# Kernel optimization log

Hardware: AMD Instinct MI355X
Metric: run time of the kernel (lower is better)

## Reference

```python
import jax, jax.numpy as jnp
import numpy as np

HIDDEN = 128
SEQ_LEN = 7
BATCH = 65536


def setup_inputs() -> dict:
    key = jax.random.key(0)
    ks = jax.random.split(key, 8)
    H = HIDDEN
    s = 1.0 / np.sqrt(H)  # PyTorch LSTM/Linear init range
    x = jax.random.normal(ks[0], (BATCH, SEQ_LEN, 1), dtype=jnp.float32)
    x0 = jax.random.uniform(ks[1], (BATCH, 1), dtype=jnp.float32)
    W_ih = jax.random.uniform(ks[2], (4 * H, 1), jnp.float32, -s, s)
    W_hh = jax.random.uniform(ks[3], (4 * H, H), jnp.float32, -s, s)
    b_ih = jax.random.uniform(ks[4], (4 * H,), jnp.float32, -s, s)
    b_hh = jax.random.uniform(ks[5], (4 * H,), jnp.float32, -s, s)
    W_out = jax.random.uniform(ks[6], (1, H), jnp.float32, -s, s)
    b_out = jax.random.uniform(ks[7], (1,), jnp.float32, -s, s)
    return {"x": x, "x0": x0, "W_ih": W_ih, "W_hh": W_hh,
            "b_ih": b_ih, "b_hh": b_hh, "W_out": W_out, "b_out": b_out}


def reference(x, x0, W_ih, W_hh, b_ih, b_hh, W_out, b_out):
    B, T, _ = x.shape
    H = W_hh.shape[1]
    # Step i consumes the output of the previous shift: x0, then x[:, 0..T-2]
    # (x[:, T-1] is assigned but never fed into the LSTM, matching the torch loop).
    xs = jnp.concatenate([x0[:, None, :], x[:, : T - 1, :]], axis=1)  # [B, T, 1]
    xs = jnp.swapaxes(xs, 0, 1)  # [T, B, 1] for scan

    h0 = jnp.zeros((B, H), dtype=x.dtype)
    c0 = jnp.zeros((B, H), dtype=x.dtype)
    bias = b_ih + b_hh  # [4H]

    def step(carry, x_t):
        h, c = carry
        # gates: [B, 4H]; PyTorch gate order is i, f, g, o
        gates = x_t @ W_ih.T + h @ W_hh.T + bias
        i_g, f_g, g_g, o_g = jnp.split(gates, 4, axis=-1)
        i_g = jax.nn.sigmoid(i_g)
        f_g = jax.nn.sigmoid(f_g)
        g_g = jnp.tanh(g_g)
        o_g = jax.nn.sigmoid(o_g)
        c_new = f_g * c + i_g * g_g
        h_new = o_g * jnp.tanh(c_new)
        pred = h_new @ W_out.T + b_out  # [B, 1]
        return (h_new, c_new), pred

    _, preds = jax.lax.scan(step, (h0, c0), xs)  # preds: [T, B, 1]
    return jnp.swapaxes(preds, 0, 1)  # [B, T, 1]
```

## Files before the change

### kernel.cpp

```cpp
#include <hip/hip_runtime.h>


#define SEQ 7
#define BT 32

typedef _Float16 half8 __attribute__((ext_vector_type(8)));
typedef float floatx4 __attribute__((ext_vector_type(4)));
typedef float floatx2 __attribute__((ext_vector_type(2)));

__device__ __forceinline__ floatx4 mfma16(half8 a, half8 b, floatx4 c) {
  return __builtin_amdgcn_mfma_f32_16x16x32_f16(a, b, c, 0, 0, 0);
}

#define LOG2E 1.4426950408889634f
#define K2 2.885390081777927f

__device__ __forceinline__ floatx2 pexp2m(floatx2 v) {
  floatx2 r;
  r.x = __builtin_amdgcn_exp2f(-v.x);
  r.y = __builtin_amdgcn_exp2f(-v.y);
  return r;
}
__device__ __forceinline__ floatx2 prcp(floatx2 v) {
  floatx2 r;
  r.x = __builtin_amdgcn_rcpf(v.x);
  r.y = __builtin_amdgcn_rcpf(v.y);
  return r;
}

__global__ void pack_kernel(const float* __restrict__ Whh,
                            const float* __restrict__ Wout,
                            _Float16* __restrict__ Bp) {
  int idx = blockIdx.x * 256 + threadIdx.x;
  if (idx < 65536) {
    int jj = idx & 7;
    int lane = (idx >> 3) & 63;
    int kk = (idx >> 9) & 3;
    int nt = idx >> 11;
    int g = nt >> 3, w = nt & 7;
    int col = lane & 15, quad = lane >> 4;
    int j = g * 128 + w * 16 + col;
    int k = 32 * kk + 8 * quad + jj;
    float S = (g == 2) ? K2 : LOG2E;
    Bp[idx] = (_Float16)(S * Whh[j * 128 + k]);
  } else {
    int pos = idx - 65536;
    int hl = pos >> 11;
    int e = pos & 2047;
    int jj = e & 7;
    int lane = (e >> 3) & 63;
    int kk = e >> 9;
    int col = lane & 15, quad = lane >> 4;
    int k = 32 * kk + 8 * quad + jj;
    float wv = Wout[k];
    _Float16 hi = (_Float16)wv;
    _Float16 v = hl ? (_Float16)(wv - (float)hi) : hi;
    Bp[idx] = (col == 0) ? v : (_Float16)0.0f;
  }
}

__launch_bounds__(512, 4)
__global__ void lstm_kernel(const float* __restrict__ x,
                            const float* __restrict__ x0,
                            const float* __restrict__ Wih,
                            const float* __restrict__ bih,
                            const float* __restrict__ bhh,
                            const float* __restrict__ boutp,
                            const _Float16* __restrict__ Bp,
                            float* __restrict__ out) {
  __shared__ _Float16 Ah[2][BT][136];
  __shared__ float xs[2][BT];
  __shared__ _Float16 Wo[4096];
  __shared__ float Twb[8][16][8];

  const int tid = threadIdx.x;
  const int w = tid >> 6;
  const int lane = tid & 63;
  const int col = lane & 15;
  const int quad = lane >> 4;
  const int rowbase = blockIdx.x * BT;

  ((half8*)Wo)[tid] = ((const half8*)(Bp + 65536))[tid];

  if (tid < 128) {
    int tw = tid >> 4, tc = tid & 15;
#pragma unroll
    for (int g = 0; g < 4; ++g) {
      int j = g * 128 + tw * 16 + tc;
      float S = (g == 2) ? K2 : LOG2E;
      Twb[tw][tc][g] = S * Wih[j];
      Twb[tw][tc][4 + g] = S * (bih[j] + bhh[j]);
    }
  }

  half8 bw[4][4];
#pragma unroll
  for (int g = 0; g < 4; ++g)
#pragma unroll
    for (int kk = 0; kk < 4; ++kk)
      bw[g][kk] =
          *(const half8*)(Bp + (((g * 8 + w) * 4 + kk) * 64 + lane) * 8);

  const float bout = boutp[0];

  floatx2 c2[2][2];
#pragma unroll
  for (int mt = 0; mt < 2; ++mt)
#pragma unroll
    for (int p = 0; p < 2; ++p) c2[mt][p] = (floatx2){0.f, 0.f};

  if (tid < BT) xs[0][tid] = x0[rowbase + tid];
  __syncthreads();

#pragma unroll 1
  for (int t = 0; t < SEQ; ++t) {
    const int cur = t & 1, nxt = cur ^ 1;

    if (t + 1 < SEQ && tid < BT) {
      xs[nxt][tid] = x[(size_t)(rowbase + tid) * 7 + t];
    }

#pragma unroll
    for (int mt = 0; mt < 2; ++mt) {
      floatx4 xq = *(const floatx4*)&xs[cur][mt * 16 + quad * 4];

      floatx4 wihv = *(volatile const floatx4*)&Twb[w][col][0];
      floatx4 biasv = *(volatile const floatx4*)&Twb[w][col][4];

      floatx4 acc[4];
#pragma unroll
      for (int g = 0; g < 4; ++g)
#pragma unroll
        for (int r = 0; r < 4; ++r)
          acc[g][r] = __builtin_fmaf(wihv[g], xq[r], biasv[g]);

      const bool dopred = (w < 2) && (mt == w);

      if (t != 0) {
        floatx4 ap = (floatx4){0.f, 0.f, 0.f, 0.f};
#pragma unroll
        for (int kk = 0; kk < 4; ++kk) {
          half8 ah =
              *(const half8*)&Ah[cur][mt * 16 + col][kk * 32 + quad * 8];
#pragma unroll
          for (int g = 0; g < 4; ++g) acc[g] = mfma16(ah, bw[g][kk], acc[g]);
          if (dopred) {
            half8 bo0 = *(const half8*)&Wo[(kk * 64 + lane) * 8];
            half8 bo1 = *(const half8*)&Wo[2048 + (kk * 64 + lane) * 8];
            ap = mfma16(ah, bo0, ap);
            ap = mfma16(ah, bo1, ap);
          }
        }
        if (dopred && col == 0) {
#pragma unroll
          for (int r = 0; r < 4; ++r)
            out[(size_t)(rowbase + mt * 16 + quad * 4 + r) * 7 + (t - 1)] =
                ap[r] + bout;
        }
      }

      const floatx2 one2 = {1.0f, 1.0f};
      const floatx2 k22 = {K2, K2};
#pragma unroll
      for (int p = 0; p < 2; ++p) {
        floatx2 Gi, Gf, Gg, Go;
        Gi.x = acc[0][2 * p];
        Gi.y = acc[0][2 * p + 1];
        Gf.x = acc[1][2 * p];
        Gf.y = acc[1][2 * p + 1];
        Gg.x = acc[2][2 * p];
        Gg.y = acc[2][2 * p + 1];
        Go.x = acc[3][2 * p];
        Go.y = acc[3][2 * p + 1];
        floatx2 A = pexp2m(Gi);
        floatx2 Bv = pexp2m(Gf);
        floatx2 Cv = pexp2m(Gg);
        floatx2 Dv = pexp2m(Go);
        floatx2 a1 = A + one2;
        floatx2 b1 = Bv + one2;
        floatx2 c1 = Cv + one2;
        floatx2 ac = a1 * c1;
        floatx2 t1 = k22 - Cv * k22;
        floatx2 num = c2[mt][p] * ac + t1 * b1;
        floatx2 den = ac * b1;
        floatx2 cn = num * prcp(den);
        c2[mt][p] = cn;
        floatx2 E = pexp2m(cn);
        floatx2 de = (Dv + one2) * (E + one2);
        floatx2 hn = (one2 - E) * prcp(de);
        Ah[nxt][mt * 16 + quad * 4 + 2 * p][w * 16 + col] = (_Float16)hn.x;
        Ah[nxt][mt * 16 + quad * 4 + 2 * p + 1][w * 16 + col] =
            (_Float16)hn.y;
      }
    }
    __syncthreads();
  }

  if (w < 2) {
    const int mt = w;
    floatx4 ap = (floatx4){0.f, 0.f, 0.f, 0.f};
#pragma unroll
    for (int kk = 0; kk < 4; ++kk) {
      half8 ah = *(const half8*)&Ah[1][mt * 16 + col][kk * 32 + quad * 8];
      half8 bo0 = *(const half8*)&Wo[(kk * 64 + lane) * 8];
      half8 bo1 = *(const half8*)&Wo[2048 + (kk * 64 + lane) * 8];
      ap = mfma16(ah, bo0, ap);
      ap = mfma16(ah, bo1, ap);
    }
    if (col == 0) {
#pragma unroll
      for (int r = 0; r < 4; ++r)
        out[(size_t)(rowbase + mt * 16 + quad * 4 + r) * 7 + 6] =
            ap[r] + bout;
    }
  }
}

extern "C" void kernel_launch(void* const* d_in, const int* in_sizes, int n_in,
                              void* d_out, int out_size, void* d_ws,
                              size_t ws_size, hipStream_t stream) {
  const float* x = (const float*)d_in[0];
  const float* x0 = (const float*)d_in[1];
  const float* Wih = (const float*)d_in[2];
  const float* Whh = (const float*)d_in[3];
  const float* bih = (const float*)d_in[4];
  const float* bhh = (const float*)d_in[5];
  const float* Wout = (const float*)d_in[6];
  const float* bout = (const float*)d_in[7];
  float* out = (float*)d_out;
  _Float16* Bp = (_Float16*)d_ws;

  pack_kernel<<<272, 256, 0, stream>>>(Whh, Wout, Bp);
  lstm_kernel<<<65536 / BT, 512, 0, stream>>>(x, x0, Wih, bih, bhh, bout, Bp,
                                              out);
}
```

Baseline: 145.7 us.

## Load x directly from global, split LDS tables, pack h stores via DPP

```diff
diff --git a/kernel.cpp b/kernel.cpp
--- a/kernel.cpp
+++ b/kernel.cpp
@@ -69,9 +69,9 @@
                             const _Float16* __restrict__ Bp,
                             float* __restrict__ out) {
   __shared__ _Float16 Ah[2][BT][136];
-  __shared__ float xs[2][BT];
   __shared__ _Float16 Wo[4096];
-  __shared__ float Twb[8][16][8];
+  __shared__ floatx4 Tw[8][16];
+  __shared__ floatx4 Tb[8][16];
 
   const int tid = threadIdx.x;
   const int w = tid >> 6;
@@ -79,17 +79,20 @@
   const int col = lane & 15;
   const int quad = lane >> 4;
   const int rowbase = blockIdx.x * BT;
+  const bool odd = (lane & 1) != 0;
 
   ((half8*)Wo)[tid] = ((const half8*)(Bp + 65536))[tid];
 
   if (tid < 128) {
     int tw = tid >> 4, tc = tid & 15;
+    float* pw = (float*)&Tw[tw][tc];
+    float* pb = (float*)&Tb[tw][tc];
 #pragma unroll
     for (int g = 0; g < 4; ++g) {
       int j = g * 128 + tw * 16 + tc;
       float S = (g == 2) ? K2 : LOG2E;
-      Twb[tw][tc][g] = S * Wih[j];
-      Twb[tw][tc][4 + g] = S * (bih[j] + bhh[j]);
+      pw[g] = S * Wih[j];
+      pb[g] = S * (bih[j] + bhh[j]);
     }
   }
 
@@ -109,30 +112,35 @@
 #pragma unroll
     for (int p = 0; p < 2; ++p) c2[mt][p] = (floatx2){0.f, 0.f};
 
-  if (tid < BT) xs[0][tid] = x0[rowbase + tid];
   __syncthreads();
 
 #pragma unroll 1
   for (int t = 0; t < SEQ; ++t) {
     const int cur = t & 1, nxt = cur ^ 1;
 
-    if (t + 1 < SEQ && tid < BT) {
-      xs[nxt][tid] = x[(size_t)(rowbase + tid) * 7 + t];
-    }
-
 #pragma unroll
     for (int mt = 0; mt < 2; ++mt) {
-      floatx4 xq = *(const floatx4*)&xs[cur][mt * 16 + quad * 4];
-
-      floatx4 wihv = *(volatile const floatx4*)&Twb[w][col][0];
-      floatx4 biasv = *(volatile const floatx4*)&Twb[w][col][4];
+      const int rowoff = rowbase + mt * 16 + quad * 4;
+      float xr0, xr1, xr2, xr3;
+      if (t == 0) {
+        xr0 = x0[rowoff + 0];
+        xr1 = x0[rowoff + 1];
+        xr2 = x0[rowoff + 2];
+        xr3 = x0[rowoff + 3];
+      } else {
+        xr0 = x[(size_t)(rowoff + 0) * 7 + (t - 1)];
+        xr1 = x[(size_t)(rowoff + 1) * 7 + (t - 1)];
+        xr2 = x[(size_t)(rowoff + 2) * 7 + (t - 1)];
+        xr3 = x[(size_t)(rowoff + 3) * 7 + (t - 1)];
+      }
+      floatx4 xq = {xr0, xr1, xr2, xr3};
+
+      floatx4 wihv = *(volatile const floatx4*)&Tw[w][col];
+      floatx4 biasv = *(volatile const floatx4*)&Tb[w][col];
 
       floatx4 acc[4];
 #pragma unroll
-      for (int g = 0; g < 4; ++g)
-#pragma unroll
-        for (int r = 0; r < 4; ++r)
-          acc[g][r] = __builtin_fmaf(wihv[g], xq[r], biasv[g]);
+      for (int g = 0; g < 4; ++g) acc[g] = xq * wihv[g] + biasv[g];
 
       const bool dopred = (w < 2) && (mt == w);
 
@@ -188,9 +196,22 @@
         floatx2 E = pexp2m(cn);
         floatx2 de = (Dv + one2) * (E + one2);
         floatx2 hn = (one2 - E) * prcp(de);
-        Ah[nxt][mt * 16 + quad * 4 + 2 * p][w * 16 + col] = (_Float16)hn.x;
-        Ah[nxt][mt * 16 + quad * 4 + 2 * p + 1][w * 16 + col] =
-            (_Float16)hn.y;
+
+        union {
+          _Float16 h[2];
+          unsigned int u;
+        } pk;
+        pk.h[0] = (_Float16)hn.x;
+        pk.h[1] = (_Float16)hn.y;
+        unsigned int t0 = pk.u;
+        unsigned int t1x = (unsigned int)__builtin_amdgcn_mov_dpp(
+            (int)t0, 0xB1, 0xF, 0xF, true);
+        unsigned int rot = (t1x >> 16) | (t1x << 16);
+        unsigned int sa = odd ? rot : t0;
+        unsigned int sb = odd ? t0 : rot;
+        unsigned int res = (sa & 0xFFFFu) | (sb & 0xFFFF0000u);
+        const int row = mt * 16 + quad * 4 + 2 * p + (odd ? 1 : 0);
+        *(unsigned int*)&Ah[nxt][row][w * 16 + (col & ~1)] = res;
       }
     }
     __syncthreads();
```

Measured after the change: 170.7 us. 17.1% more time.
